# Performance work log

Hardware: AMD Instinct MI355X
Metric: run time of the kernel (lower is better)

The kernel has to match this reference:

```python
import jax, jax.numpy as jnp
import numpy as np

S = 4          # number of species / per-species sub-modules
CUTOFF = 5.2


def _routed_mlp(feat, W, b, species_, activate=True):
    # Species-routed MLP: equivalent to per-species index_select -> m_i -> index_add.
    # Compute all species branches vectorized, then select with one-hot mask.
    h = jnp.einsum('ni,sio->nso', feat, W) + b            # [N, S, out]
    if activate:
        h = jax.nn.gelu(h)
    onehot = jax.nn.one_hot(species_, S, dtype=feat.dtype)  # [N, S]; -1 -> all-zero row
    return jnp.einsum('nso,ns->no', h, onehot)            # [N, out]


def _smooth_cutoff(d, rc):
    x = jnp.clip(d / rc, 0.0, 1.0 - 1e-6)
    f = jnp.exp(1.0 - 1.0 / (1.0 - x * x))
    return jnp.where(d < rc, f, 0.0)


def setup_inputs() -> dict:
    key = jax.random.key(0)
    ks = jax.random.split(key, 12)
    B, A, AEV, MO, NO, P = 256, 128, 1008, 256, 128, 262144
    N = B * A
    FIN = MO + NO  # 384
    species = jax.random.randint(ks[0], (B, A), 0, S, dtype=jnp.int32)
    aev = jax.random.normal(ks[1], (B, A, AEV), dtype=jnp.float32)
    atom_index12 = jax.random.randint(ks[2], (2, P), 0, N, dtype=jnp.int32)
    distances = jax.random.uniform(ks[3], (P,), dtype=jnp.float32) * CUTOFF
    total_charges = jax.random.randint(ks[4], (B,), -2, 3).astype(jnp.float32)

    def w(k, shape, fan_in):
        return jax.random.normal(k, shape, dtype=jnp.float32) / np.sqrt(fan_in)

    Wm0 = w(ks[5], (S, AEV, MO), AEV); bm0 = jnp.zeros((S, MO), jnp.float32)
    Wn0 = w(ks[6], (S, MO, NO), MO);   bn0 = jnp.zeros((S, NO), jnp.float32)
    Wm1 = w(ks[7], (S, FIN, MO), FIN); bm1 = jnp.zeros((S, MO), jnp.float32)
    Wn1 = w(ks[8], (S, MO, NO), MO);   bn1 = jnp.zeros((S, NO), jnp.float32)
    Wf  = w(ks[9], (S, FIN, 1), FIN);  bf  = jnp.zeros((S, 1), jnp.float32)
    return dict(species=species, aev=aev, atom_index12=atom_index12,
                distances=distances, total_charges=total_charges,
                Wm0=Wm0, bm0=bm0, Wn0=Wn0, bn0=bn0,
                Wm1=Wm1, bm1=bm1, Wn1=Wn1, bn1=bn1,
                Wf=Wf, bf=bf,
                factor=jnp.float32(1.0), prefactor=jnp.float32(1.0))


def reference(species, aev, atom_index12, distances, total_charges,
              Wm0, bm0, Wn0, bn0, Wm1, bm1, Wn1, bn1, Wf, bf,
              factor, prefactor):
    B, A = species.shape
    species_ = species.reshape(-1)                 # [N]
    feat = aev.reshape(-1, aev.shape[-1])          # [N, AEV]

    # ExpDistanceDecay * smooth cutoff, shared by every pass
    decay = (prefactor ** 2) * jnp.exp(-(factor ** 2) * distances) \
            * _smooth_cutoff(distances, CUTOFF)    # [P]
    idx_flat = atom_index12.reshape(-1)            # [2P] scatter targets
    idx_flip = atom_index12[::-1].reshape(-1)      # [2P] gather sources (flipud)
    decay2 = jnp.tile(decay, 2)                    # [2P]

    for (Wm, bm, Wn, bn) in ((Wm0, bm0, Wn0, bn0), (Wm1, bm1, Wn1, bn1)):
        internal = _routed_mlp(feat, Wm, bm, species_)     # [N, MO]
        neigh = _routed_mlp(internal, Wn, bn, species_)    # [N, NO]
        msgs = neigh[idx_flip] * decay2[:, None]           # [2P, NO]
        merged = jnp.zeros_like(neigh).at[idx_flat].add(msgs)
        feat = jnp.concatenate([internal, merged], axis=-1)  # [N, MO+NO]

    pre = _routed_mlp(feat, Wf, bf, species_, activate=False)[:, 0].reshape(B, A)

    dummy_mask = species != -1
    n_real = dummy_mask.sum(-1, keepdims=True).astype(pre.dtype)
    charges = pre + (total_charges - pre.sum(-1))[:, None] / n_real
    charges = jnp.where(dummy_mask, charges, 0.0)
    return species, charges, pre
```

## Files before the change

### kernel.cpp

```cpp
#include <hip/hip_runtime.h>
#include <hip/hip_bf16.h>
#include <math.h>

constexpr int S_  = 4;
constexpr int MO  = 256;
constexpr int NO  = 128;
constexpr int FIN = 384;
#define CUTOFF_F 5.2f

typedef short bf16x8 __attribute__((ext_vector_type(8)));
typedef float f32x16 __attribute__((ext_vector_type(16)));

__device__ __forceinline__ float gelu_tanh(float x) {
    float u = 0.7978845608028654f * (x + 0.044715f * x * x * x);
    return 0.5f * x * (1.0f + tanhf(u));
}
__device__ __forceinline__ unsigned short f2bf(float x) {
    unsigned u = __float_as_uint(x);
    u = (u + 0x7fffu + ((u >> 16) & 1u)) >> 16;
    return (unsigned short)u;
}
__device__ __forceinline__ float bf2f(unsigned short h) {
    return __uint_as_float(((unsigned)h) << 16);
}

__global__ void decay_kernel(const float* __restrict__ dist, const float* __restrict__ fa_,
                             const float* __restrict__ pf_, float* __restrict__ decay, int P) {
    int i = blockIdx.x * blockDim.x + threadIdx.x;
    if (i >= P) return;
    float fa = fa_[0], pf = pf_[0];
    float d = dist[i];
    float x = fminf(fmaxf(d / CUTOFF_F, 0.0f), 1.0f - 1e-6f);
    float f = expf(1.0f - 1.0f / (1.0f - x * x));
    float w = (d < CUTOFF_F) ? f : 0.0f;
    decay[i] = pf * pf * expf(-(fa * fa) * d) * w;
}

__global__ void species_hist(const int* __restrict__ sp, int* __restrict__ bhist, int N) {
    __shared__ int h[S_];
    int t = threadIdx.x, b = blockIdx.x;
    if (t < S_) h[t] = 0;
    __syncthreads();
    int i = b * 256 + t;
    if (i < N) {
        int s = sp[i];
        if (s >= 0 && s < S_) atomicAdd(&h[s], 1);
    }
    __syncthreads();
    if (t < S_) bhist[b * 4 + t] = h[t];
}
__global__ void species_scan(const int* __restrict__ bhist, int* __restrict__ cnt,
                             int* __restrict__ pbase, int nb) {
    if (threadIdx.x != 0) return;
    int tot[S_];
    for (int s = 0; s < S_; ++s) {
        int sum = 0;
        for (int b = 0; b < nb; ++b) sum += bhist[b * 4 + s];
        tot[s] = sum;
    }
    int off = 0;
    for (int s = 0; s < S_; ++s) { cnt[s] = tot[s]; cnt[4 + s] = off; off += tot[s]; }
    for (int s = 0; s < S_; ++s) {
        int run = cnt[4 + s];
        for (int b = 0; b < nb; ++b) { pbase[b * 4 + s] = run; run += bhist[b * 4 + s]; }
    }
}
__global__ void species_fill(const int* __restrict__ sp, const int* __restrict__ pbase,
                             int* __restrict__ perm, int N) {
    __shared__ int cur[S_];
    int t = threadIdx.x, b = blockIdx.x;
    if (t < S_) cur[t] = pbase[b * 4 + t];
    __syncthreads();
    int i = b * 256 + t;
    if (i < N) {
        int s = sp[i];
        if (s >= 0 && s < S_) {
            int pos = atomicAdd(&cur[s], 1);
            perm[pos] = i;
        }
    }
}

__global__ void edge_count(const int* __restrict__ ai, int* __restrict__ degree, int P2) {
    int e = blockIdx.x * blockDim.x + threadIdx.x;
    if (e < P2) atomicAdd(&degree[ai[e]], 1);
}
__global__ void scan_rowptr(const int* __restrict__ degree, int* __restrict__ rowptr,
                            int* __restrict__ cursor, int N) {
    __shared__ int lds[1024];
    int t = threadIdx.x;
    int per = N / 1024;
    int base = t * per;
    int sum = 0;
    for (int i = 0; i < per; ++i) sum += degree[base + i];
    lds[t] = sum;
    __syncthreads();
    int v = sum;
    for (int ofs = 1; ofs < 1024; ofs <<= 1) {
        int add = (t >= ofs) ? lds[t - ofs] : 0;
        __syncthreads();
        v += add;
        lds[t] = v;
        __syncthreads();
    }
    int run = v - sum;
    for (int i = 0; i < per; ++i) {
        int d = degree[base + i];
        rowptr[base + i] = run;
        cursor[base + i] = run;
        run += d;
    }
    if (t == 1023) rowptr[N] = run;
}
__global__ void edge_fill(const int* __restrict__ ai, const float* __restrict__ decay,
                          int* __restrict__ cursor, int* __restrict__ col,
                          float* __restrict__ wgt, int P) {
    int e = blockIdx.x * blockDim.x + threadIdx.x;
    if (e >= 2 * P) return;
    int p = (e < P) ? e : e - P;
    int dst = ai[e];
    int src = (e < P) ? ai[P + p] : ai[p];
    int pos = atomicAdd(&cursor[dst], 1);
    col[pos] = src;
    wgt[pos] = decay[p];
}

__global__ void cast_aev(const float* __restrict__ in, unsigned short* __restrict__ outb, int total4) {
    int i = blockIdx.x * blockDim.x + threadIdx.x;
    if (i >= total4) return;
    float4 v = ((const float4*)in)[i];
    ushort4 o; o.x = f2bf(v.x); o.y = f2bf(v.y); o.z = f2bf(v.z); o.w = f2bf(v.w);
    ((ushort4*)outb)[i] = o;
}

__global__ void transpose_cast(const float* __restrict__ W, unsigned short* __restrict__ Wt,
                               int K, int NC) {
    __shared__ float tile[32][33];
    int s = blockIdx.z;
    int nb = blockIdx.x * 32, kb = blockIdx.y * 32;
    int tx = threadIdx.x & 31, ty = threadIdx.x >> 5;
    const float* Wb = W + (size_t)s * K * NC;
    unsigned short* Wo = Wt + (size_t)s * NC * K;
#pragma unroll
    for (int i = 0; i < 4; ++i) {
        int k = kb + ty + i * 8;
        tile[ty + i * 8][tx] = (k < K) ? Wb[(size_t)k * NC + nb + tx] : 0.0f;
    }
    __syncthreads();
#pragma unroll
    for (int i = 0; i < 4; ++i) {
        int n = nb + ty + i * 8;
        int k = kb + tx;
        if (k < K) Wo[(size_t)n * K + k] = f2bf(tile[tx][ty + i * 8]);
    }
}

template<int K, int NC, bool ACT>
__launch_bounds__(256, 2)
__global__ void mfma_gemm(const unsigned short* __restrict__ A, int lda,
                          const unsigned short* __restrict__ Wt,
                          const float* __restrict__ bias,
                          unsigned short* __restrict__ C, int ldc,
                          const int* __restrict__ cnt, const int* __restrict__ perm) {
    const int s = blockIdx.z;
    const int count = cnt[s];
    const int row0 = blockIdx.y * 64;
    if (row0 >= count) return;
    const int off = cnt[4 + s];
    const int c0 = blockIdx.x * 128;

    __shared__ unsigned short As[64 * 40];
    __shared__ unsigned short Bs[128 * 40];
    __shared__ int rix[64];

    const int t = threadIdx.x;
    const int lane = t & 63, wave = t >> 6;
    const int wm = wave >> 1, wn = wave & 1;
    const int l31 = lane & 31, lhi = lane >> 5;

    if (t < 64) {
        int ri = row0 + t;
        rix[t] = (ri < count) ? perm[off + ri] : -1;
    }
    __syncthreads();

    const int ra = t >> 2, qa = t & 3;
    const int rbr = t >> 1, hb = t & 1;
    const int gA = rix[ra];
    const unsigned short* Arow = (gA >= 0) ? (A + (size_t)gA * lda) : nullptr;
    const unsigned short* wrow = Wt + ((size_t)s * NC + c0 + rbr) * K;

    f32x16 acc0 = {}, acc1 = {};
    const uint4 z4 = {0, 0, 0, 0};

    for (int k0 = 0; k0 < K; k0 += 32) {
        const int ka = k0 + qa * 8;
        uint4 av = z4;
        if (ka < K && Arow) av = *(const uint4*)(Arow + ka);
        const int kb = k0 + hb * 16;
        uint4 b0 = z4, b1 = z4;
        if (kb < K) {
            const uint4* q = (const uint4*)(wrow + kb);
            b0 = q[0]; b1 = q[1];
        }
        __syncthreads();
        *(uint4*)(&As[ra * 40 + qa * 8]) = av;
        *(uint4*)(&Bs[rbr * 40 + hb * 16])     = b0;
        *(uint4*)(&Bs[rbr * 40 + hb * 16 + 8]) = b1;
        __syncthreads();
#pragma unroll
        for (int ks = 0; ks < 2; ++ks) {
            const int ch = (ks * 2 + lhi) * 8;
            bf16x8 fa  = *(const bf16x8*)(&As[(wm * 32 + l31) * 40 + ch]);
            bf16x8 fb0 = *(const bf16x8*)(&Bs[(wn * 64 +  0 + l31) * 40 + ch]);
            bf16x8 fb1 = *(const bf16x8*)(&Bs[(wn * 64 + 32 + l31) * 40 + ch]);
            acc0 = __builtin_amdgcn_mfma_f32_32x32x16_bf16(fa, fb0, acc0, 0, 0, 0);
            acc1 = __builtin_amdgcn_mfma_f32_32x32x16_bf16(fa, fb1, acc1, 0, 0, 0);
        }
    }

    const float* bp = bias + s * NC;
    auto store = [&](const f32x16& vv, int fn) {
        int col = c0 + wn * 64 + fn * 32 + l31;
        float bia = bp[col];
#pragma unroll
        for (int reg = 0; reg < 16; ++reg) {
            int frow = (reg & 3) + 8 * (reg >> 2) + 4 * lhi;
            int r = wm * 32 + frow;
            int g = rix[r];
            if (g >= 0) {
                float x = vv[reg] + bia;
                if (ACT) x = gelu_tanh(x);
                C[(size_t)g * ldc + col] = f2bf(x);
            }
        }
    };
    store(acc0, 0); store(acc1, 1);
}

__global__ void gather_rows0(const unsigned short* __restrict__ neigh,
                             const int* __restrict__ rowptr, const int* __restrict__ col,
                             const float* __restrict__ wgt,
                             unsigned short* __restrict__ featout) {
    int row = blockIdx.x * 4 + (threadIdx.x >> 6);
    int lane = threadIdx.x & 63;
    int b = rowptr[row], e = rowptr[row + 1];
    int j = lane * 2;
    float a0 = 0.f, a1 = 0.f, c0 = 0.f, c1 = 0.f;
    int i = b;
    for (; i + 1 < e; i += 2) {
        int s0 = col[i], s1 = col[i + 1];
        float w0 = wgt[i], w1 = wgt[i + 1];
        unsigned p0 = *(const unsigned*)(neigh + (size_t)s0 * NO + j);
        unsigned p1 = *(const unsigned*)(neigh + (size_t)s1 * NO + j);
        a0 += bf2f((unsigned short)(p0 & 0xffffu)) * w0;
        a1 += bf2f((unsigned short)(p0 >> 16)) * w0;
        c0 += bf2f((unsigned short)(p1 & 0xffffu)) * w1;
        c1 += bf2f((unsigned short)(p1 >> 16)) * w1;
    }
    if (i < e) {
        int s0 = col[i];
        float w0 = wgt[i];
        unsigned p0 = *(const unsigned*)(neigh + (size_t)s0 * NO + j);
        a0 += bf2f((unsigned short)(p0 & 0xffffu)) * w0;
        a1 += bf2f((unsigned short)(p0 >> 16)) * w0;
    }
    a0 += c0; a1 += c1;
    unsigned short o0 = f2bf(a0), o1 = f2bf(a1);
    *(unsigned*)(featout + (size_t)row * FIN + MO + j) = ((unsigned)o1 << 16) | (unsigned)o0;
}

__global__ void gather_final(const unsigned short* __restrict__ neigh,
                             const int* __restrict__ rowptr, const int* __restrict__ col,
                             const float* __restrict__ wgt,
                             const unsigned short* __restrict__ int1,
                             const float* __restrict__ Wf, const float* __restrict__ bfb,
                             const int* __restrict__ species, float* __restrict__ out, int N) {
    int w = blockIdx.x * 4 + (threadIdx.x >> 6);
    int lane = threadIdx.x & 63;
    int s = species[w];
    float acc = 0.0f;
    if (s >= 0) {
        const float* wp = Wf + (size_t)s * FIN;
        int b = rowptr[w], e = rowptr[w + 1];
        int j = lane * 2;
        float a0 = 0.f, a1 = 0.f, c0 = 0.f, c1 = 0.f;
        int i = b;
        for (; i + 1 < e; i += 2) {
            int s0 = col[i], s1 = col[i + 1];
            float w0 = wgt[i], w1 = wgt[i + 1];
            unsigned p0 = *(const unsigned*)(neigh + (size_t)s0 * NO + j);
            unsigned p1 = *(const unsigned*)(neigh + (size_t)s1 * NO + j);
            a0 += bf2f((unsigned short)(p0 & 0xffffu)) * w0;
            a1 += bf2f((unsigned short)(p0 >> 16)) * w0;
            c0 += bf2f((unsigned short)(p1 & 0xffffu)) * w1;
            c1 += bf2f((unsigned short)(p1 >> 16)) * w1;
        }
        if (i < e) {
            int s0 = col[i];
            float w0 = wgt[i];
            unsigned p0 = *(const unsigned*)(neigh + (size_t)s0 * NO + j);
            a0 += bf2f((unsigned short)(p0 & 0xffffu)) * w0;
            a1 += bf2f((unsigned short)(p0 >> 16)) * w0;
        }
        a0 += c0; a1 += c1;
        acc = a0 * wp[MO + j] + a1 * wp[MO + j + 1];
        const unsigned short* ip = int1 + (size_t)w * MO + lane * 4;
        ushort4 iv = *(const ushort4*)ip;
        const float* wq = wp + lane * 4;
        acc += bf2f(iv.x) * wq[0] + bf2f(iv.y) * wq[1] + bf2f(iv.z) * wq[2] + bf2f(iv.w) * wq[3];
    }
    for (int o = 32; o > 0; o >>= 1) acc += __shfl_down(acc, o, 64);
    if (lane == 0) {
        float pre = (s >= 0) ? (acc + bfb[s]) : 0.0f;
        out[2 * (size_t)N + w] = pre;
        out[w] = (float)s;
    }
}

__global__ void charges_kernel(const float* __restrict__ pre_buf, const int* __restrict__ species,
                               const float* __restrict__ tc, float* __restrict__ out, int N, int A) {
    int b = blockIdx.x;
    int a = threadIdx.x;
    int idx = b * A + a;
    float pre = pre_buf[idx];
    int sp = species[idx];
    bool mask = (sp != -1);
    float v = pre;
    int c = mask ? 1 : 0;
    for (int o = 32; o > 0; o >>= 1) {
        v += __shfl_down(v, o, 64);
        c += __shfl_down(c, o, 64);
    }
    __shared__ float ssum[2];
    __shared__ int scnt[2];
    int wid = threadIdx.x >> 6;
    if ((threadIdx.x & 63) == 0) { ssum[wid] = v; scnt[wid] = c; }
    __syncthreads();
    float total = ssum[0] + ssum[1];
    int nreal = scnt[0] + scnt[1];
    float ch = pre + (tc[b] - total) / (float)max(nreal, 1);
    out[(size_t)N + idx] = mask ? ch : 0.0f;
}

extern "C" void kernel_launch(void* const* d_in, const int* in_sizes, int n_in,
                              void* d_out, int out_size, void* d_ws, size_t ws_size,
                              hipStream_t stream) {
    const int*   species = (const int*)d_in[0];
    const float* aev     = (const float*)d_in[1];
    const int*   ai      = (const int*)d_in[2];
    const float* dist    = (const float*)d_in[3];
    const float* tc      = (const float*)d_in[4];
    const float* Wm0 = (const float*)d_in[5];  const float* bm0 = (const float*)d_in[6];
    const float* Wn0 = (const float*)d_in[7];  const float* bn0 = (const float*)d_in[8];
    const float* Wm1 = (const float*)d_in[9];  const float* bm1 = (const float*)d_in[10];
    const float* Wn1 = (const float*)d_in[11]; const float* bn1 = (const float*)d_in[12];
    const float* Wf  = (const float*)d_in[13]; const float* bf  = (const float*)d_in[14];
    const float* factor    = (const float*)d_in[15];
    const float* prefactor = (const float*)d_in[16];

    const int N   = in_sizes[0];
    const int AEV = in_sizes[1] / N;
    const int P   = in_sizes[3];
    const int B   = in_sizes[4];
    const int A   = N / B;

    float* out = (float*)d_out;

    char* base = (char*)d_ws;
    size_t o = 0;
    auto take = [&](size_t bytes) -> char* {
        o = (o + 255) & ~(size_t)255;
        char* p = base + o; o += bytes; return p;
    };
    unsigned short* feat1_bf = (unsigned short*)take((size_t)N * FIN * 2);
    unsigned short* int1_bf  = (unsigned short*)take((size_t)N * MO * 2);
    char* region             = take((size_t)N * AEV * 2);
    unsigned short* aev_bf   = (unsigned short*)region;
    unsigned short* neigh_bf = (unsigned short*)region;
    size_t roff = ((size_t)N * NO * 2 + 255) & ~(size_t)255;
    int* rowptr = (int*)(region + roff);  roff += (size_t)(N + 1) * 4; roff = (roff + 255) & ~(size_t)255;
    int* cursor = (int*)(region + roff);  roff += (size_t)N * 4;       roff = (roff + 255) & ~(size_t)255;
    int* degree = (int*)(region + roff);  roff += (size_t)N * 4;       roff = (roff + 255) & ~(size_t)255;
    int* ecol   = (int*)(region + roff);  roff += (size_t)2 * P * 4;   roff = (roff + 255) & ~(size_t)255;
    float* ewgt = (float*)(region + roff);
    float* decay = (float*)take((size_t)P * 4);
    unsigned short* Wm0t = (unsigned short*)take((size_t)S_ * MO * AEV * 2);
    unsigned short* Wn0t = (unsigned short*)take((size_t)S_ * NO * MO * 2);
    unsigned short* Wm1t = (unsigned short*)take((size_t)S_ * MO * FIN * 2);
    unsigned short* Wn1t = (unsigned short*)take((size_t)S_ * NO * MO * 2);
    int* perm  = (int*)take((size_t)N * 4);
    int* cnt   = (int*)take(64);
    const int nb = (N + 255) / 256;
    int* bhist = (int*)take((size_t)nb * 4 * 4);
    int* pbase = (int*)take((size_t)nb * 4 * 4);

    species_hist<<<nb, 256, 0, stream>>>(species, bhist, N);
    species_scan<<<1, 64, 0, stream>>>(bhist, cnt, pbase, nb);
    species_fill<<<nb, 256, 0, stream>>>(species, pbase, perm, N);
    decay_kernel<<<(P + 255) / 256, 256, 0, stream>>>(dist, factor, prefactor, decay, P);

    const int tot4 = N * (AEV / 4);
    cast_aev<<<(tot4 + 255) / 256, 256, 0, stream>>>(aev, aev_bf, tot4);
    transpose_cast<<<dim3(MO / 32, (AEV + 31) / 32, S_), 256, 0, stream>>>(Wm0, Wm0t, AEV, MO);
    transpose_cast<<<dim3(NO / 32, MO / 32, S_), 256, 0, stream>>>(Wn0, Wn0t, MO, NO);
    transpose_cast<<<dim3(MO / 32, FIN / 32, S_), 256, 0, stream>>>(Wm1, Wm1t, FIN, MO);
    transpose_cast<<<dim3(NO / 32, MO / 32, S_), 256, 0, stream>>>(Wn1, Wn1t, MO, NO);

    const int rb = (N + 63) / 64;

    mfma_gemm<1008, 256, true><<<dim3(2, rb, S_), 256, 0, stream>>>(
        aev_bf, AEV, Wm0t, bm0, feat1_bf, FIN, cnt, perm);

    hipMemsetAsync(degree, 0, (size_t)N * 4, stream);
    edge_count<<<(2 * P + 255) / 256, 256, 0, stream>>>(ai, degree, 2 * P);
    scan_rowptr<<<1, 1024, 0, stream>>>(degree, rowptr, cursor, N);
    edge_fill<<<(2 * P + 255) / 256, 256, 0, stream>>>(ai, decay, cursor, ecol, ewgt, P);

    mfma_gemm<256, 128, true><<<dim3(1, rb, S_), 256, 0, stream>>>(
        feat1_bf, FIN, Wn0t, bn0, neigh_bf, NO, cnt, perm);
    gather_rows0<<<N / 4, 256, 0, stream>>>(neigh_bf, rowptr, ecol, ewgt, feat1_bf);

    mfma_gemm<384, 256, true><<<dim3(2, rb, S_), 256, 0, stream>>>(
        feat1_bf, FIN, Wm1t, bm1, int1_bf, MO, cnt, perm);
    mfma_gemm<256, 128, true><<<dim3(1, rb, S_), 256, 0, stream>>>(
        int1_bf, MO, Wn1t, bn1, neigh_bf, NO, cnt, perm);

    gather_final<<<N / 4, 256, 0, stream>>>(
        neigh_bf, rowptr, ecol, ewgt, int1_bf, Wf, bf, species, out, N);
    charges_kernel<<<B, A, 0, stream>>>(out + 2 * (size_t)N, species, tc, out, N, A);
}
```

Before: 629.9 us.

## Fuse decay into edge_fill, add 32-row GEMM for neighbor layers, unroll gathers

Drops the separate decay kernel and its buffer by computing the decay weight inline in edge_fill. Adds a 32-row-tile MFMA GEMM variant for the two K=256 to 128-column neighbor projections, meant to raise block count and occupancy on these small GEMMs. The two gather kernels now unroll by four edges to keep more independent loads in flight. The smaller tile re-reads the weights more often, and unrolling adds register pressure.

```diff
diff --git a/kernel.cpp b/kernel.cpp
--- a/kernel.cpp
+++ b/kernel.cpp
@@ -23,17 +23,11 @@
 __device__ __forceinline__ float bf2f(unsigned short h) {
     return __uint_as_float(((unsigned)h) << 16);
 }
-
-__global__ void decay_kernel(const float* __restrict__ dist, const float* __restrict__ fa_,
-                             const float* __restrict__ pf_, float* __restrict__ decay, int P) {
-    int i = blockIdx.x * blockDim.x + threadIdx.x;
-    if (i >= P) return;
-    float fa = fa_[0], pf = pf_[0];
-    float d = dist[i];
+__device__ __forceinline__ float decay_of(float d, float fa, float pf) {
     float x = fminf(fmaxf(d / CUTOFF_F, 0.0f), 1.0f - 1e-6f);
     float f = expf(1.0f - 1.0f / (1.0f - x * x));
     float w = (d < CUTOFF_F) ? f : 0.0f;
-    decay[i] = pf * pf * expf(-(fa * fa) * d) * w;
+    return pf * pf * expf(-(fa * fa) * d) * w;
 }
 
 __global__ void species_hist(const int* __restrict__ sp, int* __restrict__ bhist, int N) {
@@ -112,7 +106,8 @@
     }
     if (t == 1023) rowptr[N] = run;
 }
-__global__ void edge_fill(const int* __restrict__ ai, const float* __restrict__ decay,
+__global__ void edge_fill(const int* __restrict__ ai, const float* __restrict__ dist,
+                          const float* __restrict__ fa_, const float* __restrict__ pf_,
                           int* __restrict__ cursor, int* __restrict__ col,
                           float* __restrict__ wgt, int P) {
     int e = blockIdx.x * blockDim.x + threadIdx.x;
@@ -122,7 +117,7 @@
     int src = (e < P) ? ai[P + p] : ai[p];
     int pos = atomicAdd(&cursor[dst], 1);
     col[pos] = src;
-    wgt[pos] = decay[p];
+    wgt[pos] = decay_of(dist[p], fa_[0], pf_[0]);
 }
 
 __global__ void cast_aev(const float* __restrict__ in, unsigned short* __restrict__ outb, int total4) {
@@ -238,6 +233,83 @@
     store(acc0, 0); store(acc1, 1);
 }
 
+template<int K, bool ACT>
+__launch_bounds__(256, 2)
+__global__ void mfma_gemm32(const unsigned short* __restrict__ A, int lda,
+                            const unsigned short* __restrict__ Wt,
+                            const float* __restrict__ bias,
+                            unsigned short* __restrict__ C, int ldc,
+                            const int* __restrict__ cnt, const int* __restrict__ perm) {
+    const int s = blockIdx.z;
+    const int count = cnt[s];
+    const int row0 = blockIdx.y * 32;
+    if (row0 >= count) return;
+    const int off = cnt[4 + s];
+    constexpr int NC = 128;
+
+    __shared__ unsigned short As[32 * 40];
+    __shared__ unsigned short Bs[128 * 40];
+    __shared__ int rix[32];
+
+    const int t = threadIdx.x;
+    const int lane = t & 63, wave = t >> 6;
+    const int l31 = lane & 31, lhi = lane >> 5;
+
+    if (t < 32) {
+        int ri = row0 + t;
+        rix[t] = (ri < count) ? perm[off + ri] : -1;
+    }
+    __syncthreads();
+
+    const int ra = t >> 3, qa = t & 7;
+    const int rbr = t >> 1, hb = t & 1;
+    const int gA = rix[ra];
+    const unsigned short* Arow = (gA >= 0) ? (A + (size_t)gA * lda) : nullptr;
+    const unsigned short* wrow = Wt + ((size_t)s * NC + rbr) * K;
+
+    f32x16 acc = {};
+    const uint4 z4 = {0, 0, 0, 0};
+    const uint2 z2 = {0, 0};
+
+    for (int k0 = 0; k0 < K; k0 += 32) {
+        const int ka = k0 + qa * 4;
+        uint2 av = z2;
+        if (ka < K && Arow) av = *(const uint2*)(Arow + ka);
+        const int kb = k0 + hb * 16;
+        uint4 b0 = z4, b1 = z4;
+        if (kb < K) {
+            const uint4* q = (const uint4*)(wrow + kb);
+            b0 = q[0]; b1 = q[1];
+        }
+        __syncthreads();
+        *(uint2*)(&As[ra * 40 + qa * 4]) = av;
+        *(uint4*)(&Bs[rbr * 40 + hb * 16])     = b0;
+        *(uint4*)(&Bs[rbr * 40 + hb * 16 + 8]) = b1;
+        __syncthreads();
+#pragma unroll
+        for (int ks = 0; ks < 2; ++ks) {
+            const int ch = (ks * 2 + lhi) * 8;
+            bf16x8 fa = *(const bf16x8*)(&As[l31 * 40 + ch]);
+            bf16x8 fb = *(const bf16x8*)(&Bs[(wave * 32 + l31) * 40 + ch]);
+            acc = __builtin_amdgcn_mfma_f32_32x32x16_bf16(fa, fb, acc, 0, 0, 0);
+        }
+    }
+
+    const float* bp = bias + s * NC;
+    int col = wave * 32 + l31;
+    float bia = bp[col];
+#pragma unroll
+    for (int reg = 0; reg < 16; ++reg) {
+        int frow = (reg & 3) + 8 * (reg >> 2) + 4 * lhi;
+        int g = rix[frow];
+        if (g >= 0) {
+            float x = acc[reg] + bia;
+            if (ACT) x = gelu_tanh(x);
+            C[(size_t)g * ldc + col] = f2bf(x);
+        }
+    }
+}
+
 __global__ void gather_rows0(const unsigned short* __restrict__ neigh,
                              const int* __restrict__ rowptr, const int* __restrict__ col,
                              const float* __restrict__ wgt,
@@ -248,17 +320,19 @@
     int j = lane * 2;
     float a0 = 0.f, a1 = 0.f, c0 = 0.f, c1 = 0.f;
     int i = b;
-    for (; i + 1 < e; i += 2) {
-        int s0 = col[i], s1 = col[i + 1];
-        float w0 = wgt[i], w1 = wgt[i + 1];
+    for (; i + 3 < e; i += 4) {
+        int s0 = col[i], s1 = col[i + 1], s2 = col[i + 2], s3 = col[i + 3];
+        float w0 = wgt[i], w1 = wgt[i + 1], w2 = wgt[i + 2], w3 = wgt[i + 3];
         unsigned p0 = *(const unsigned*)(neigh + (size_t)s0 * NO + j);
         unsigned p1 = *(const unsigned*)(neigh + (size_t)s1 * NO + j);
-        a0 += bf2f((unsigned short)(p0 & 0xffffu)) * w0;
-        a1 += bf2f((unsigned short)(p0 >> 16)) * w0;
-        c0 += bf2f((unsigned short)(p1 & 0xffffu)) * w1;
-        c1 += bf2f((unsigned short)(p1 >> 16)) * w1;
-    }
-    if (i < e) {
+        unsigned p2 = *(const unsigned*)(neigh + (size_t)s2 * NO + j);
+        unsigned p3 = *(const unsigned*)(neigh + (size_t)s3 * NO + j);
+        a0 += bf2f((unsigned short)(p0 & 0xffffu)) * w0 + bf2f((unsigned short)(p2 & 0xffffu)) * w2;
+        a1 += bf2f((unsigned short)(p0 >> 16)) * w0 + bf2f((unsigned short)(p2 >> 16)) * w2;
+        c0 += bf2f((unsigned short)(p1 & 0xffffu)) * w1 + bf2f((unsigned short)(p3 & 0xffffu)) * w3;
+        c1 += bf2f((unsigned short)(p1 >> 16)) * w1 + bf2f((unsigned short)(p3 >> 16)) * w3;
+    }
+    for (; i < e; ++i) {
         int s0 = col[i];
         float w0 = wgt[i];
         unsigned p0 = *(const unsigned*)(neigh + (size_t)s0 * NO + j);
@@ -286,17 +360,19 @@
         int j = lane * 2;
         float a0 = 0.f, a1 = 0.f, c0 = 0.f, c1 = 0.f;
         int i = b;
-        for (; i + 1 < e; i += 2) {
-            int s0 = col[i], s1 = col[i + 1];
-            float w0 = wgt[i], w1 = wgt[i + 1];
+        for (; i + 3 < e; i += 4) {
+            int s0 = col[i], s1 = col[i + 1], s2 = col[i + 2], s3 = col[i + 3];
+            float w0 = wgt[i], w1 = wgt[i + 1], w2 = wgt[i + 2], w3 = wgt[i + 3];
             unsigned p0 = *(const unsigned*)(neigh + (size_t)s0 * NO + j);
             unsigned p1 = *(const unsigned*)(neigh + (size_t)s1 * NO + j);
-            a0 += bf2f((unsigned short)(p0 & 0xffffu)) * w0;
-            a1 += bf2f((unsigned short)(p0 >> 16)) * w0;
-            c0 += bf2f((unsigned short)(p1 & 0xffffu)) * w1;
-            c1 += bf2f((unsigned short)(p1 >> 16)) * w1;
-        }
-        if (i < e) {
+            unsigned p2 = *(const unsigned*)(neigh + (size_t)s2 * NO + j);
+            unsigned p3 = *(const unsigned*)(neigh + (size_t)s3 * NO + j);
+            a0 += bf2f((unsigned short)(p0 & 0xffffu)) * w0 + bf2f((unsigned short)(p2 & 0xffffu)) * w2;
+            a1 += bf2f((unsigned short)(p0 >> 16)) * w0 + bf2f((unsigned short)(p2 >> 16)) * w2;
+            c0 += bf2f((unsigned short)(p1 & 0xffffu)) * w1 + bf2f((unsigned short)(p3 & 0xffffu)) * w3;
+            c1 += bf2f((unsigned short)(p1 >> 16)) * w1 + bf2f((unsigned short)(p3 >> 16)) * w3;
+        }
+        for (; i < e; ++i) {
             int s0 = col[i];
             float w0 = wgt[i];
             unsigned p0 = *(const unsigned*)(neigh + (size_t)s0 * NO + j);
@@ -384,7 +460,6 @@
     int* degree = (int*)(region + roff);  roff += (size_t)N * 4;       roff = (roff + 255) & ~(size_t)255;
     int* ecol   = (int*)(region + roff);  roff += (size_t)2 * P * 4;   roff = (roff + 255) & ~(size_t)255;
     float* ewgt = (float*)(region + roff);
-    float* decay = (float*)take((size_t)P * 4);
     unsigned short* Wm0t = (unsigned short*)take((size_t)S_ * MO * AEV * 2);
     unsigned short* Wn0t = (unsigned short*)take((size_t)S_ * NO * MO * 2);
     unsigned short* Wm1t = (unsigned short*)take((size_t)S_ * MO * FIN * 2);
@@ -398,7 +473,6 @@
     species_hist<<<nb, 256, 0, stream>>>(species, bhist, N);
     species_scan<<<1, 64, 0, stream>>>(bhist, cnt, pbase, nb);
     species_fill<<<nb, 256, 0, stream>>>(species, pbase, perm, N);
-    decay_kernel<<<(P + 255) / 256, 256, 0, stream>>>(dist, factor, prefactor, decay, P);
 
     const int tot4 = N * (AEV / 4);
     cast_aev<<<(tot4 + 255) / 256, 256, 0, stream>>>(aev, aev_bf, tot4);
@@ -407,7 +481,8 @@
     transpose_cast<<<dim3(MO / 32, FIN / 32, S_), 256, 0, stream>>>(Wm1, Wm1t, FIN, MO);
     transpose_cast<<<dim3(NO / 32, MO / 32, S_), 256, 0, stream>>>(Wn1, Wn1t, MO, NO);
 
-    const int rb = (N + 63) / 64;
+    const int rb  = (N + 63) / 64;
+    const int rb32 = (N + 31) / 32;
 
     mfma_gemm<1008, 256, true><<<dim3(2, rb, S_), 256, 0, stream>>>(
         aev_bf, AEV, Wm0t, bm0, feat1_bf, FIN, cnt, perm);
@@ -415,15 +490,16 @@
     hipMemsetAsync(degree, 0, (size_t)N * 4, stream);
     edge_count<<<(2 * P + 255) / 256, 256, 0, stream>>>(ai, degree, 2 * P);
     scan_rowptr<<<1, 1024, 0, stream>>>(degree, rowptr, cursor, N);
-    edge_fill<<<(2 * P + 255) / 256, 256, 0, stream>>>(ai, decay, cursor, ecol, ewgt, P);
-
-    mfma_gemm<256, 128, true><<<dim3(1, rb, S_), 256, 0, stream>>>(
+    edge_fill<<<(2 * P + 255) / 256, 256, 0, stream>>>(ai, dist, factor, prefactor,
+                                                       cursor, ecol, ewgt, P);
+
+    mfma_gemm32<256, true><<<dim3(1, rb32, S_), 256, 0, stream>>>(
         feat1_bf, FIN, Wn0t, bn0, neigh_bf, NO, cnt, perm);
     gather_rows0<<<N / 4, 256, 0, stream>>>(neigh_bf, rowptr, ecol, ewgt, feat1_bf);
 
     mfma_gemm<384, 256, true><<<dim3(2, rb, S_), 256, 0, stream>>>(
         feat1_bf, FIN, Wm1t, bm1, int1_bf, MO, cnt, perm);
-    mfma_gemm<256, 128, true><<<dim3(1, rb, S_), 256, 0, stream>>>(
+    mfma_gemm32<256, true><<<dim3(1, rb32, S_), 256, 0, stream>>>(
         int1_bf, MO, Wn1t, bn1, neigh_bf, NO, cnt, perm);
 
     gather_final<<<N / 4, 256, 0, stream>>>(
```

New measurement: 610.9 us. -3.0%, faster.
